# Performance work log

Measured on AMD Instinct MI355X. Metric: run time of the kernel, lower is better.

The kernel has to match this reference:

```python
import jax, jax.numpy as jnp
import numpy as np
from jax import lax

B_, L_, C_IN = 32, 1024, 3
D_MODEL, D_STATE, D_CONV, EXPAND = 256, 16, 4, 2
D_INNER = EXPAND * D_MODEL           # 512
DT_RANK = D_MODEL // 16              # 16
N_HEADS, N_CLASS = 8, 10
LN_EPS = 1e-5


def _pos_emb(L, d):
    pos = np.arange(L, dtype=np.float32)[:, None]
    div = np.exp(np.arange(0, d, 2, dtype=np.float32) * (-np.log(10000.0) / d))
    pe = np.zeros((L, d), np.float32)
    pe[:, 0::2] = np.sin(pos * div)
    pe[:, 1::2] = np.cos(pos * div)
    return jnp.asarray(pe)


def setup_inputs() -> dict:
    key = jax.random.key(0)
    ks = jax.random.split(key, 12)
    f = lambda k, shp, s: jax.random.normal(k, shp, jnp.float32) * s
    return {
        'x_enc': f(ks[0], (B_, L_, C_IN), 1.0),
        'x_mark_enc': jnp.ones((B_, L_), jnp.float32),
        'conv_emb_w': f(ks[1], (D_MODEL, C_IN, 3), (2.0 / (C_IN * 3)) ** 0.5),
        'in_proj_w': f(ks[2], (2 * D_INNER, D_MODEL), D_MODEL ** -0.5),
        'conv1d_w': f(ks[3], (D_INNER, 1, D_CONV), D_CONV ** -0.5),
        'conv1d_b': f(ks[4], (D_INNER,), 0.02),
        'x_proj_w': f(ks[5], (DT_RANK + 2 * D_STATE, D_INNER), D_INNER ** -0.5),
        'dt_proj_w': f(ks[6], (D_INNER, DT_RANK), DT_RANK ** -0.5),
        'dt_proj_b': f(ks[7], (D_INNER,), 0.1) - 2.0,
        'A_log': jnp.log(jnp.tile(jnp.arange(1, D_STATE + 1, dtype=jnp.float32), (D_INNER, 1))),
        'D': jnp.ones((D_INNER,), jnp.float32),
        'out_proj_w': f(ks[8], (D_MODEL, D_INNER), D_INNER ** -0.5),
        'ln_g': jnp.ones((D_MODEL,), jnp.float32),
        'ln_b': jnp.zeros((D_MODEL,), jnp.float32),
        'out_w': f(ks[9], (N_CLASS, D_MODEL), D_MODEL ** -0.5),
        'attn_w': f(ks[10], (N_HEADS, D_MODEL), 0.02),
        'attn_b': jnp.ones((N_HEADS,), jnp.float32),
    }


def _forward(x_enc, x_mark_enc, conv_emb_w, in_proj_w, conv1d_w, conv1d_b,
             x_proj_w, dt_proj_w, dt_proj_b, A_log, D, out_proj_w,
             ln_g, ln_b, out_w, attn_w, attn_b):
    silu = jax.nn.silu
    # --- embedding: Conv1d 'same' with replicate padding + sinusoidal PE ---
    xp = jnp.pad(x_enc, ((0, 0), (1, 1), (0, 0)), mode='edge')      # k=3 -> pad (1,1)
    x = lax.conv_general_dilated(xp.transpose(0, 2, 1), conv_emb_w, (1,), 'VALID',
                                 dimension_numbers=('NCH', 'OIH', 'NCH')).transpose(0, 2, 1)
    x = x + _pos_emb(L_, D_MODEL)[None]                              # (B,L,D)

    # --- Mamba_TimeVariant (standard Mamba selective scan) ---
    xz = jnp.einsum('bld,ed->ble', x, in_proj_w)                     # (B,L,2*Din)
    xin, z = xz[..., :D_INNER], xz[..., D_INNER:]
    # depthwise causal conv, kernel D_CONV
    xc = jnp.pad(xin.transpose(0, 2, 1), ((0, 0), (0, 0), (D_CONV - 1, 0)))
    xc = lax.conv_general_dilated(xc, conv1d_w, (1,), 'VALID',
                                  feature_group_count=D_INNER,
                                  dimension_numbers=('NCH', 'OIH', 'NCH'))
    xc = silu(xc.transpose(0, 2, 1) + conv1d_b)                      # (B,L,Din)

    dbl = jnp.einsum('bld,ed->ble', xc, x_proj_w)                    # (B,L,dt_rank+2*N)
    dtr = dbl[..., :DT_RANK]
    Bm = dbl[..., DT_RANK:DT_RANK + D_STATE]                         # (B,L,N)
    Cm = dbl[..., DT_RANK + D_STATE:]                                # (B,L,N)
    dt = jax.nn.softplus(jnp.einsum('blr,dr->bld', dtr, dt_proj_w) + dt_proj_b)
    A = -jnp.exp(A_log)                                              # (Din,N)

    def step(h, inp):
        dt_t, B_t, C_t, x_t = inp                                    # (B,Din),(B,N),(B,N),(B,Din)
        dA = jnp.exp(dt_t[..., None] * A)                            # (B,Din,N)
        h = dA * h + dt_t[..., None] * B_t[:, None, :] * x_t[..., None]
        y = jnp.einsum('bdn,bn->bd', h, C_t)
        return h, y

    h0 = jnp.zeros((B_, D_INNER, D_STATE), xc.dtype)
    inputs = (dt.transpose(1, 0, 2), Bm.transpose(1, 0, 2),
              Cm.transpose(1, 0, 2), xc.transpose(1, 0, 2))
    _, ys = lax.scan(step, h0, inputs)                               # (L,B,Din)
    y = ys.transpose(1, 0, 2) + xc * D                               # skip via D
    y = y * silu(z)
    m = jnp.einsum('bld,ed->ble', y, out_proj_w)                     # (B,L,Dmodel)

    # LayerNorm + SiLU
    mu = m.mean(-1, keepdims=True)
    var = ((m - mu) ** 2).mean(-1, keepdims=True)
    m = (m - mu) * lax.rsqrt(var + LN_EPS) * ln_g + ln_b
    m = silu(m)

    # classification head
    logit = jnp.einsum('bld,cd->blc', m, out_w) * x_mark_enc[..., None]
    s = jnp.einsum('bld,hd->blh', m, attn_w) + attn_b                # (B,L,H)
    w = jax.nn.softmax(jnp.max(s, axis=2, keepdims=True), axis=1)    # (B,L,1)
    return (logit * w).sum(1)                                        # (B,num_class)


def reference(x_enc, x_mark_enc, conv_emb_w, in_proj_w, conv1d_w, conv1d_b,
              x_proj_w, dt_proj_w, dt_proj_b, A_log, D, out_proj_w,
              ln_g, ln_b, out_w, attn_w, attn_b):
    return _forward(x_enc, x_mark_enc, conv_emb_w, in_proj_w, conv1d_w, conv1d_b,
                    x_proj_w, dt_proj_w, dt_proj_b, A_log, D, out_proj_w,
                    ln_g, ln_b, out_w, attn_w, attn_b)
```

## Files before the change

kernel.cpp:

```cpp
#include <hip/hip_runtime.h>
#include <hip/hip_bf16.h>
#include <math.h>

#define B_  32
#define L_  1024
#define CIN 3
#define DM  256
#define DI  512
#define NST 16
#define NH  8
#define NC  10
#define M_TOT (B_*L_)

typedef unsigned short u16;
typedef __attribute__((ext_vector_type(8))) short bf16x8;
typedef __attribute__((ext_vector_type(4))) float f32x4;

static __device__ __forceinline__ float sigmoidf_(float x) {
    return 1.0f / (1.0f + __expf(-x));
}
static __device__ __forceinline__ u16 f2bf(float f) {
    unsigned int u = __float_as_uint(f);
    return (u16)((u + 0x7FFF + ((u >> 16) & 1)) >> 16);
}
static __device__ __forceinline__ float bf2f(u16 u) {
    return __uint_as_float(((unsigned int)u) << 16);
}

static __device__ __forceinline__ void reduce16_quad(float& a, float& b,
                                                     float& c, float& d) {
    asm volatile(
        "s_nop 1\n\t"
        "v_add_f32 %0, %0, %0 quad_perm:[1,0,3,2] row_mask:0xf bank_mask:0xf\n\t"
        "v_add_f32 %1, %1, %1 quad_perm:[1,0,3,2] row_mask:0xf bank_mask:0xf\n\t"
        "v_add_f32 %2, %2, %2 quad_perm:[1,0,3,2] row_mask:0xf bank_mask:0xf\n\t"
        "v_add_f32 %3, %3, %3 quad_perm:[1,0,3,2] row_mask:0xf bank_mask:0xf\n\t"
        "v_add_f32 %0, %0, %0 quad_perm:[2,3,0,1] row_mask:0xf bank_mask:0xf\n\t"
        "v_add_f32 %1, %1, %1 quad_perm:[2,3,0,1] row_mask:0xf bank_mask:0xf\n\t"
        "v_add_f32 %2, %2, %2 quad_perm:[2,3,0,1] row_mask:0xf bank_mask:0xf\n\t"
        "v_add_f32 %3, %3, %3 quad_perm:[2,3,0,1] row_mask:0xf bank_mask:0xf\n\t"
        "v_add_f32 %0, %0, %0 row_ror:4 row_mask:0xf bank_mask:0xf\n\t"
        "v_add_f32 %1, %1, %1 row_ror:4 row_mask:0xf bank_mask:0xf\n\t"
        "v_add_f32 %2, %2, %2 row_ror:4 row_mask:0xf bank_mask:0xf\n\t"
        "v_add_f32 %3, %3, %3 row_ror:4 row_mask:0xf bank_mask:0xf\n\t"
        "v_add_f32 %0, %0, %0 row_ror:8 row_mask:0xf bank_mask:0xf\n\t"
        "v_add_f32 %1, %1, %1 row_ror:8 row_mask:0xf bank_mask:0xf\n\t"
        "v_add_f32 %2, %2, %2 row_ror:8 row_mask:0xf bank_mask:0xf\n\t"
        "v_add_f32 %3, %3, %3 row_ror:8 row_mask:0xf bank_mask:0xf\n\t"
        : "+v"(a), "+v"(b), "+v"(c), "+v"(d));
}

__global__ __launch_bounds__(256) void k_cvt(const float* __restrict__ in,
        u16* __restrict__ out) {
    int i = (blockIdx.x * 256 + threadIdx.x) * 4;
    float4 v = *(const float4*)(in + i);
    ushort4 o;
    o.x = f2bf(v.x); o.y = f2bf(v.y); o.z = f2bf(v.z); o.w = f2bf(v.w);
    *(ushort4*)(out + i) = o;
}

__global__ __launch_bounds__(256) void k_embed(const float* __restrict__ xe,
        const float* __restrict__ w, u16* __restrict__ x) {
    int bl = blockIdx.x;
    int l = bl & (L_-1);
    int b = bl >> 10;
    int d = threadIdx.x;
    const float* xb = xe + (size_t)b * L_ * CIN;
    int t0 = l > 0 ? l-1 : 0;
    int t2 = l < L_-1 ? l+1 : L_-1;
    const float* w3 = w + d*9;
    float acc = 0.f;
    #pragma unroll
    for (int i = 0; i < 3; ++i) {
        acc += xb[t0*3+i] * w3[i*3+0];
        acc += xb[l *3+i] * w3[i*3+1];
        acc += xb[t2*3+i] * w3[i*3+2];
    }
    int j = d >> 1;
    float div = expf((float)(2*j) * (-logf(10000.0f)/(float)DM));
    float ang = (float)l * div;
    acc += (d & 1) ? cosf(ang) : sinf(ang);
    x[(size_t)bl*DM + d] = f2bf(acc);
}

#define GST 40
__global__ __launch_bounds__(256) void k_gemm_mfma(
        const u16* __restrict__ A, const u16* __restrict__ W,
        float* __restrict__ O1, u16* __restrict__ O2b,
        int M, int N, int K, int S) {
    __shared__ u16 As[128*GST];
    __shared__ u16 Bs[128*GST];
    int tid = threadIdx.x;
    int row0 = blockIdx.y * 128, col0 = blockIdx.x * 128;
    int wave = tid >> 6, lane = tid & 63;
    int wr = (wave >> 1) * 64, wc = (wave & 1) * 64;
    int l16 = lane & 15, kl = lane >> 4;
    int srow = tid >> 1, skh = (tid & 1) * 16;
    const u16* Ag = A + (size_t)(row0 + srow) * K + skh;
    const u16* Wg = W + (size_t)(col0 + srow) * K + skh;

    f32x4 acc[4][4];
    #pragma unroll
    for (int m = 0; m < 4; ++m)
        #pragma unroll
        for (int n = 0; n < 4; ++n)
            acc[m][n] = (f32x4){0.f, 0.f, 0.f, 0.f};

    for (int k0 = 0; k0 < K; k0 += 32) {
        uint4 a0 = *(const uint4*)(Ag + k0);
        uint4 a1 = *(const uint4*)(Ag + k0 + 8);
        uint4 b0 = *(const uint4*)(Wg + k0);
        uint4 b1 = *(const uint4*)(Wg + k0 + 8);
        __syncthreads();
        *(uint4*)&As[srow*GST + skh]     = a0;
        *(uint4*)&As[srow*GST + skh + 8] = a1;
        *(uint4*)&Bs[srow*GST + skh]     = b0;
        *(uint4*)&Bs[srow*GST + skh + 8] = b1;
        __syncthreads();
        bf16x8 af[4], bf[4];
        #pragma unroll
        for (int m = 0; m < 4; ++m)
            af[m] = *(const bf16x8*)&As[(wr + m*16 + l16)*GST + kl*8];
        #pragma unroll
        for (int n = 0; n < 4; ++n)
            bf[n] = *(const bf16x8*)&Bs[(wc + n*16 + l16)*GST + kl*8];
        #pragma unroll
        for (int m = 0; m < 4; ++m)
            #pragma unroll
            for (int n = 0; n < 4; ++n)
                acc[m][n] = __builtin_amdgcn_mfma_f32_16x16x32_bf16(
                                af[m], bf[n], acc[m][n], 0, 0, 0);
    }

    #pragma unroll
    for (int m = 0; m < 4; ++m) {
        int rbase = row0 + wr + m*16 + kl*4;
        #pragma unroll
        for (int n = 0; n < 4; ++n) {
            int col = col0 + wc + n*16 + l16;
            #pragma unroll
            for (int r = 0; r < 4; ++r) {
                float v = acc[m][n][r];
                if (col < S) O1[(size_t)(rbase + r)*S + col] = v;
                else         O2b[(size_t)(rbase + r)*(N - S) + (col - S)] = f2bf(v);
            }
        }
    }
}

__global__ __launch_bounds__(256) void k_conv(const float* __restrict__ xin,
        const float* __restrict__ w, const float* __restrict__ bias,
        float* __restrict__ xc) {
    size_t i4 = (size_t)blockIdx.x * 256 + threadIdx.x;
    int d4 = (int)(i4 & (DI/4 - 1)) * 4;
    size_t m = i4 >> 7;
    int l = (int)(m & (L_-1));
    float4 wv0 = *(const float4*)(w + (size_t)(d4+0)*4);
    float4 wv1 = *(const float4*)(w + (size_t)(d4+1)*4);
    float4 wv2 = *(const float4*)(w + (size_t)(d4+2)*4);
    float4 wv3 = *(const float4*)(w + (size_t)(d4+3)*4);
    float W[4][4] = {{wv0.x,wv0.y,wv0.z,wv0.w},{wv1.x,wv1.y,wv1.z,wv1.w},
                     {wv2.x,wv2.y,wv2.z,wv2.w},{wv3.x,wv3.y,wv3.z,wv3.w}};
    float4 acc = *(const float4*)(bias + d4);
    #pragma unroll
    for (int k = 0; k < 4; ++k) {
        int t = l + k - 3;
        if (t >= 0) {
            float4 xv = *(const float4*)(xin + (m + k - 3)*DI + d4);
            acc.x = fmaf(xv.x, W[0][k], acc.x);
            acc.y = fmaf(xv.y, W[1][k], acc.y);
            acc.z = fmaf(xv.z, W[2][k], acc.z);
            acc.w = fmaf(xv.w, W[3][k], acc.w);
        }
    }
    float4 r;
    r.x = acc.x * sigmoidf_(acc.x);
    r.y = acc.y * sigmoidf_(acc.y);
    r.z = acc.z * sigmoidf_(acc.z);
    r.w = acc.w * sigmoidf_(acc.w);
    *(float4*)(xc + m*DI + d4) = r;
}

#define XBM 128
#define XBK 16
__global__ __launch_bounds__(256) void k_xproj(const float* __restrict__ xc,
        const float* __restrict__ wp, float* __restrict__ dbl) {
    __shared__ float As[XBK][XBM];
    __shared__ float Ws[XBK][48];
    int tid = threadIdx.x;
    int row0 = blockIdx.x * XBM;
    int lr = tid >> 1;
    int lk = (tid & 1) * 8;
    int we = tid >> 2;
    int wk = (tid & 3) * 4;
    int tx = tid & 15;
    int ty = tid >> 4;
    float acc[8][3];
    #pragma unroll
    for (int i = 0; i < 8; ++i)
        #pragma unroll
        for (int j = 0; j < 3; ++j) acc[i][j] = 0.f;

    for (int k0 = 0; k0 < DI; k0 += XBK) {
        float4 a0 = *(const float4*)(xc + (size_t)(row0+lr)*DI + k0 + lk);
        float4 a1 = *(const float4*)(xc + (size_t)(row0+lr)*DI + k0 + lk + 4);
        float4 w0 = make_float4(0.f,0.f,0.f,0.f);
        if (tid < 192) w0 = *(const float4*)(wp + (size_t)we*DI + k0 + wk);
        __syncthreads();
        As[lk+0][lr]=a0.x; As[lk+1][lr]=a0.y; As[lk+2][lr]=a0.z; As[lk+3][lr]=a0.w;
        As[lk+4][lr]=a1.x; As[lk+5][lr]=a1.y; As[lk+6][lr]=a1.z; As[lk+7][lr]=a1.w;
        if (tid < 192) {
            Ws[wk+0][we]=w0.x; Ws[wk+1][we]=w0.y; Ws[wk+2][we]=w0.z; Ws[wk+3][we]=w0.w;
        }
        __syncthreads();
        #pragma unroll
        for (int k = 0; k < XBK; ++k) {
            float4 av0 = *(const float4*)&As[k][ty*8];
            float4 av1 = *(const float4*)&As[k][ty*8+4];
            float w0_ = Ws[k][tx*3+0];
            float w1_ = Ws[k][tx*3+1];
            float w2_ = Ws[k][tx*3+2];
            float ar[8] = {av0.x,av0.y,av0.z,av0.w,av1.x,av1.y,av1.z,av1.w};
            #pragma unroll
            for (int i = 0; i < 8; ++i) {
                acc[i][0] = fmaf(ar[i], w0_, acc[i][0]);
                acc[i][1] = fmaf(ar[i], w1_, acc[i][1]);
                acc[i][2] = fmaf(ar[i], w2_, acc[i][2]);
            }
        }
    }
    #pragma unroll
    for (int i = 0; i < 8; ++i) {
        size_t r = row0 + ty*8 + i;
        #pragma unroll
        for (int j = 0; j < 3; ++j)
            dbl[r*48 + tx*3 + j] = acc[i][j];
    }
}

__global__ __launch_bounds__(256) void k_dtproj(const float* __restrict__ dbl,
        const float* __restrict__ dtw, const float* __restrict__ dtb,
        float* __restrict__ dt) {
    __shared__ float wl[DI][17];
    __shared__ float rl[32][16];
    size_t m0 = (size_t)blockIdx.x * 32;
    for (int i = threadIdx.x; i < DI*16; i += 256)
        wl[i >> 4][i & 15] = dtw[i];
    for (int i = threadIdx.x; i < 32*16; i += 256)
        rl[i >> 4][i & 15] = dbl[(m0 + (i>>4))*48 + (i & 15)];
    __syncthreads();
    float b0 = dtb[threadIdx.x];
    float b1 = dtb[256 + threadIdx.x];
    for (int mm = 0; mm < 32; ++mm) {
        #pragma unroll
        for (int half = 0; half < 2; ++half) {
            int d = half*256 + threadIdx.x;
            float acc = half ? b1 : b0;
            #pragma unroll
            for (int r = 0; r < 16; ++r)
                acc = fmaf(rl[mm][r], wl[d][r], acc);
            float sp = fmaxf(acc, 0.f) + log1pf(__expf(-fabsf(acc)));
            dt[(m0+mm)*DI + d] = sp;
        }
    }
}

#define SCAN_T 64
__global__ __launch_bounds__(256) void k_scan(const float* __restrict__ dt,
        const float* __restrict__ xc, const float* __restrict__ dbl,
        const float* __restrict__ A_log, const float* __restrict__ Dp,
        const u16* __restrict__ zbf, u16* __restrict__ ybf) {
    __shared__ float4 sq4[SCAN_T*17];

    int tid = threadIdx.x;
    int ch = tid >> 4;
    int n  = tid & 15;
    int d0 = blockIdx.x * 16;
    int b  = blockIdx.y;
    int d  = d0 + ch;
    float Avl2 = -expf(A_log[(size_t)d*NST + n]) * 1.44269504f;
    float h = 0.f;
    size_t base = (size_t)b * L_;

    int st = tid >> 2;
    int sc = (tid & 3) * 4;
    float4 Dv = *(const float4*)(Dp + d0 + sc);

    for (int t0 = 0; t0 < L_; t0 += SCAN_T) {
        __syncthreads();
        {
            size_t row = base + t0 + st;
            float4 dtv = *(const float4*)(dt + row*DI + d0 + sc);
            float4 xv  = *(const float4*)(xc + row*DI + d0 + sc);
            ushort4 zv4 = *(const ushort4*)(zbf + row*DI + d0 + sc);
            float z0 = bf2f(zv4.x), z1 = bf2f(zv4.y);
            float z2 = bf2f(zv4.z), z3 = bf2f(zv4.w);
            float g0 = z0 * sigmoidf_(z0);
            float g1 = z1 * sigmoidf_(z1);
            float g2 = z2 * sigmoidf_(z2);
            float g3 = z3 * sigmoidf_(z3);
            sq4[st*17 + sc+0] = make_float4(dtv.x, dtv.x*xv.x, xv.x*Dv.x*g0, g0);
            sq4[st*17 + sc+1] = make_float4(dtv.y, dtv.y*xv.y, xv.y*Dv.y*g1, g1);
            sq4[st*17 + sc+2] = make_float4(dtv.z, dtv.z*xv.z, xv.z*Dv.z*g2, g2);
            sq4[st*17 + sc+3] = make_float4(dtv.w, dtv.w*xv.w, xv.w*Dv.w*g3, g3);
        }
        __syncthreads();

        for (int tt = 0; tt < SCAN_T; tt += 16) {
            float Br[16], Cr[16];
            #pragma unroll
            for (int j = 0; j < 16; ++j) {
                size_t r48 = (base + t0 + tt + j) * 48;
                Br[j] = dbl[r48 + 16 + n];
                Cr[j] = dbl[r48 + 32 + n];
            }
            #pragma unroll
            for (int j4 = 0; j4 < 4; ++j4) {
                int tb = tt + j4*4;
                float4 q0 = sq4[(tb+0)*17 + ch];
                float4 q1 = sq4[(tb+1)*17 + ch];
                float4 q2 = sq4[(tb+2)*17 + ch];
                float4 q3 = sq4[(tb+3)*17 + ch];
                float dA;
                dA = exp2f(q0.x * Avl2);
                h = fmaf(dA, h, q0.y * Br[j4*4+0]);
                float p0 = h * Cr[j4*4+0];
                dA = exp2f(q1.x * Avl2);
                h = fmaf(dA, h, q1.y * Br[j4*4+1]);
                float p1 = h * Cr[j4*4+1];
                dA = exp2f(q2.x * Avl2);
                h = fmaf(dA, h, q2.y * Br[j4*4+2]);
                float p2 = h * Cr[j4*4+2];
                dA = exp2f(q3.x * Avl2);
                h = fmaf(dA, h, q3.y * Br[j4*4+3]);
                float p3 = h * Cr[j4*4+3];
                reduce16_quad(p0, p1, p2, p3);
                if (n == 0) {
                    size_t row = base + t0 + tb;
                    ybf[(row+0)*DI + d] = f2bf(fmaf(p0, q0.w, q0.z));
                    ybf[(row+1)*DI + d] = f2bf(fmaf(p1, q1.w, q1.z));
                    ybf[(row+2)*DI + d] = f2bf(fmaf(p2, q2.w, q2.z));
                    ybf[(row+3)*DI + d] = f2bf(fmaf(p3, q3.w, q3.z));
                }
            }
        }
    }
}

__global__ __launch_bounds__(256) void k_lnsilu(float* __restrict__ m,
        const float* __restrict__ g, const float* __restrict__ bta) {
    size_t row = (size_t)blockIdx.x*4 + (threadIdx.x >> 6);
    int lane = threadIdx.x & 63;
    float4 v = *(const float4*)(m + row*DM + lane*4);
    float s = v.x + v.y + v.z + v.w;
    #pragma unroll
    for (int o = 32; o > 0; o >>= 1) s += __shfl_xor(s, o);
    float mu = s * (1.0f/DM);
    float4 c = make_float4(v.x-mu, v.y-mu, v.z-mu, v.w-mu);
    float s2 = c.x*c.x + c.y*c.y + c.z*c.z + c.w*c.w;
    #pragma unroll
    for (int o = 32; o > 0; o >>= 1) s2 += __shfl_xor(s2, o);
    float rstd = 1.0f / sqrtf(s2 * (1.0f/DM) + 1e-5f);
    float4 gv = *(const float4*)(g + lane*4);
    float4 bv = *(const float4*)(bta + lane*4);
    float o0 = c.x*rstd*gv.x + bv.x;
    float o1 = c.y*rstd*gv.y + bv.y;
    float o2 = c.z*rstd*gv.z + bv.z;
    float o3 = c.w*rstd*gv.w + bv.w;
    float4 r;
    r.x = o0 * sigmoidf_(o0);
    r.y = o1 * sigmoidf_(o1);
    r.z = o2 * sigmoidf_(o2);
    r.w = o3 * sigmoidf_(o3);
    *(float4*)(m + row*DM + lane*4) = r;
}

#define HBK 32
__global__ __launch_bounds__(256) void k_heads18(const float* __restrict__ m,
        const float* __restrict__ aw, const float* __restrict__ ow,
        float* __restrict__ r18) {
    __shared__ float As[128][36];
    __shared__ float Ws[18][36];
    int tid = threadIdx.x;
    int row0 = blockIdx.x * 128;
    int r = tid >> 1, ch = tid & 1, cb = ch * 9;
    int sr = tid >> 1, sk = (tid & 1) * 16;
    float acc[9];
    #pragma unroll
    for (int c = 0; c < 9; ++c) acc[c] = 0.f;

    for (int k0 = 0; k0 < DM; k0 += HBK) {
        float4 a[4];
        #pragma unroll
        for (int q = 0; q < 4; ++q)
            a[q] = *(const float4*)(m + (size_t)(row0+sr)*DM + k0 + sk + q*4);
        float4 wv = make_float4(0.f,0.f,0.f,0.f);
        int wc = tid >> 3, wk = (tid & 7) * 4;
        if (tid < 144) {
            const float* wsrc = (wc < NH) ? (aw + wc*DM) : (ow + (wc-NH)*DM);
            wv = *(const float4*)(wsrc + k0 + wk);
        }
        __syncthreads();
        #pragma unroll
        for (int q = 0; q < 4; ++q)
            *(float4*)&As[sr][sk + q*4] = a[q];
        if (tid < 144)
            *(float4*)&Ws[wc][wk] = wv;
        __syncthreads();
        #pragma unroll
        for (int k4 = 0; k4 < HBK/4; ++k4) {
            float4 av = *(const float4*)&As[r][k4*4];
            #pragma unroll
            for (int c = 0; c < 9; ++c) {
                float4 w4 = *(const float4*)&Ws[cb + c][k4*4];
                acc[c] += av.x*w4.x + av.y*w4.y + av.z*w4.z + av.w*w4.w;
            }
        }
        __syncthreads();
    }
    #pragma unroll
    for (int c = 0; c < 9; ++c)
        r18[(size_t)(row0 + r)*18 + cb + c] = acc[c];
}

__global__ __launch_bounds__(256) void k_final(const float* __restrict__ r18,
        const float* __restrict__ ab, const float* __restrict__ xmark,
        float* __restrict__ out) {
    __shared__ float e[L_];
    __shared__ float red[256];
    int b = blockIdx.x;
    int tid = threadIdx.x;
    float abr[NH];
    #pragma unroll
    for (int j = 0; j < NH; ++j) abr[j] = ab[j];
    float mx = -1e30f;
    for (int l = tid; l < L_; l += 256) {
        const float* rr = r18 + ((size_t)b*L_ + l)*18;
        float sm = rr[0] + abr[0];
        #pragma unroll
        for (int j = 1; j < NH; ++j) sm = fmaxf(sm, rr[j] + abr[j]);
        e[l] = sm;
        mx = fmaxf(mx, sm);
    }
    #pragma unroll
    for (int o = 32; o > 0; o >>= 1) mx = fmaxf(mx, __shfl_xor(mx, o));
    red[tid] = mx;
    __syncthreads();
    mx = fmaxf(fmaxf(red[0], red[64]), fmaxf(red[128], red[192]));
    __syncthreads();
    float ssum = 0.f;
    for (int l = tid; l < L_; l += 256) {
        float ev = __expf(e[l] - mx);
        e[l] = ev;
        ssum += ev;
    }
    #pragma unroll
    for (int o = 32; o > 0; o >>= 1) ssum += __shfl_xor(ssum, o);
    if ((tid & 63) == 0) red[tid >> 6] = ssum;
    __syncthreads();
    float inv = 1.0f / (red[0]+red[1]+red[2]+red[3]);
    float acc[NC];
    #pragma unroll
    for (int c = 0; c < NC; ++c) acc[c] = 0.f;
    for (int l = tid; l < L_; l += 256) {
        float wl = e[l] * xmark[(size_t)b*L_ + l];
        const float* lg = r18 + ((size_t)b*L_ + l)*18 + NH;
        #pragma unroll
        for (int c = 0; c < NC; ++c) acc[c] = fmaf(wl, lg[c], acc[c]);
    }
    __syncthreads();
    for (int c = 0; c < NC; ++c) {
        red[tid] = acc[c];
        __syncthreads();
        if (tid < 64) {
            float s2 = red[tid]+red[tid+64]+red[tid+128]+red[tid+192];
            #pragma unroll
            for (int o = 32; o > 0; o >>= 1) s2 += __shfl_xor(s2, o);
            if (tid == 0) out[(size_t)b*NC + c] = s2 * inv;
        }
        __syncthreads();
    }
}

extern "C" void kernel_launch(void* const* d_in, const int* in_sizes, int n_in,
                              void* d_out, int out_size, void* d_ws, size_t ws_size,
                              hipStream_t stream) {
    const float* x_enc  = (const float*)d_in[0];
    const float* x_mark = (const float*)d_in[1];
    const float* cemb_w = (const float*)d_in[2];
    const float* inp_w  = (const float*)d_in[3];
    const float* c1_w   = (const float*)d_in[4];
    const float* c1_b   = (const float*)d_in[5];
    const float* xp_w   = (const float*)d_in[6];
    const float* dtp_w  = (const float*)d_in[7];
    const float* dtp_b  = (const float*)d_in[8];
    const float* A_log  = (const float*)d_in[9];
    const float* Dp     = (const float*)d_in[10];
    const float* outp_w = (const float*)d_in[11];
    const float* ln_g   = (const float*)d_in[12];
    const float* ln_b   = (const float*)d_in[13];
    const float* out_w  = (const float*)d_in[14];
    const float* attn_w = (const float*)d_in[15];
    const float* attn_b = (const float*)d_in[16];
    float* out = (float*)d_out;

    char* ws = (char*)d_ws;
    size_t o = 0;
    u16*   xbf  = (u16*)(ws + o);  o += (size_t)M_TOT*DM*2;
    float* xin  = (float*)(ws + o); o += (size_t)M_TOT*DI*4;
    u16*   zbf  = (u16*)(ws + o);  o += (size_t)M_TOT*DI*2;
    float* xc   = (float*)(ws + o); o += (size_t)M_TOT*DI*4;
    u16*   ybf  = (u16*)(ws + o);  o += (size_t)M_TOT*DI*2;
    float* dbl  = (float*)(ws + o); o += (size_t)M_TOT*48*4;
    u16*   wbfi = (u16*)(ws + o);  o += (size_t)2*DI*DM*2;
    u16*   wbfo = (u16*)(ws + o);  o += (size_t)DM*DI*2;
    float* r18  = (float*)(ws + o); o += (size_t)M_TOT*18*4;
    float* dt = xin;
    float* mm = xc;

    k_cvt   <<<(2*DI*DM)/1024, 256, 0, stream>>>(inp_w, wbfi);
    k_cvt   <<<(DM*DI)/1024, 256, 0, stream>>>(outp_w, wbfo);
    k_embed <<<M_TOT, 256, 0, stream>>>(x_enc, cemb_w, xbf);
    k_gemm_mfma<<<dim3(8, M_TOT/128), 256, 0, stream>>>(xbf, wbfi, xin, zbf,
                                                        M_TOT, 2*DI, DM, DI);
    k_conv  <<<(M_TOT*DI/4)/256, 256, 0, stream>>>(xin, c1_w, c1_b, xc);
    k_xproj <<<M_TOT/XBM, 256, 0, stream>>>(xc, xp_w, dbl);
    k_dtproj<<<M_TOT/32, 256, 0, stream>>>(dbl, dtp_w, dtp_b, dt);
    k_scan  <<<dim3(DI/16, B_), 256, 0, stream>>>(dt, xc, dbl, A_log, Dp, zbf, ybf);
    k_gemm_mfma<<<dim3(2, M_TOT/128), 256, 0, stream>>>(ybf, wbfo, mm, zbf,
                                                        M_TOT, DM, DI, DM);
    k_lnsilu<<<M_TOT/4, 256, 0, stream>>>(mm, ln_g, ln_b);
    k_heads18<<<M_TOT/128, 256, 0, stream>>>(mm, attn_w, out_w, r18);
    k_final <<<B_, 256, 0, stream>>>(r18, attn_b, x_mark, out);
}
```

Measured before the change: 475.0 us.

## Transpose B/C projections to state-major layout and spread scan output stores

```diff
diff --git a/kernel.cpp b/kernel.cpp
--- a/kernel.cpp
+++ b/kernel.cpp
@@ -184,7 +184,8 @@
 #define XBM 128
 #define XBK 16
 __global__ __launch_bounds__(256) void k_xproj(const float* __restrict__ xc,
-        const float* __restrict__ wp, float* __restrict__ dbl) {
+        const float* __restrict__ wp, float* __restrict__ dbl,
+        float* __restrict__ BT, float* __restrict__ CT) {
     __shared__ float As[XBK][XBM];
     __shared__ float Ws[XBK][48];
     int tid = threadIdx.x;
@@ -233,8 +234,13 @@
     for (int i = 0; i < 8; ++i) {
         size_t r = row0 + ty*8 + i;
         #pragma unroll
-        for (int j = 0; j < 3; ++j)
-            dbl[r*48 + tx*3 + j] = acc[i][j];
+        for (int j = 0; j < 3; ++j) {
+            int c = tx*3 + j;
+            float v = acc[i][j];
+            if (c < 16)      dbl[r*48 + c] = v;
+            else if (c < 32) BT[(size_t)(c-16)*M_TOT + r] = v;
+            else             CT[(size_t)(c-32)*M_TOT + r] = v;
+        }
     }
 }
 
@@ -267,9 +273,10 @@
 
 #define SCAN_T 64
 __global__ __launch_bounds__(256) void k_scan(const float* __restrict__ dt,
-        const float* __restrict__ xc, const float* __restrict__ dbl,
-        const float* __restrict__ A_log, const float* __restrict__ Dp,
-        const u16* __restrict__ zbf, u16* __restrict__ ybf) {
+        const float* __restrict__ xc, const float* __restrict__ BT,
+        const float* __restrict__ CT, const float* __restrict__ A_log,
+        const float* __restrict__ Dp, const u16* __restrict__ zbf,
+        u16* __restrict__ ybf) {
     __shared__ float4 sq4[SCAN_T*17];
 
     int tid = threadIdx.x;
@@ -281,6 +288,8 @@
     float Avl2 = -expf(A_log[(size_t)d*NST + n]) * 1.44269504f;
     float h = 0.f;
     size_t base = (size_t)b * L_;
+    const float* BTn = BT + (size_t)n * M_TOT + base;
+    const float* CTn = CT + (size_t)n * M_TOT + base;
 
     int st = tid >> 2;
     int sc = (tid & 3) * 4;
@@ -307,13 +316,13 @@
         __syncthreads();
 
         for (int tt = 0; tt < SCAN_T; tt += 16) {
-            float Br[16], Cr[16];
-            #pragma unroll
-            for (int j = 0; j < 16; ++j) {
-                size_t r48 = (base + t0 + tt + j) * 48;
-                Br[j] = dbl[r48 + 16 + n];
-                Cr[j] = dbl[r48 + 32 + n];
+            float4 Bv[4], Cv[4];
+            #pragma unroll
+            for (int q = 0; q < 4; ++q) {
+                Bv[q] = *(const float4*)(BTn + t0 + tt + q*4);
+                Cv[q] = *(const float4*)(CTn + t0 + tt + q*4);
             }
+            float yreg = 0.f;
             #pragma unroll
             for (int j4 = 0; j4 < 4; ++j4) {
                 int tb = tt + j4*4;
@@ -321,28 +330,33 @@
                 float4 q1 = sq4[(tb+1)*17 + ch];
                 float4 q2 = sq4[(tb+2)*17 + ch];
                 float4 q3 = sq4[(tb+3)*17 + ch];
+                const float* Bp = (const float*)&Bv[j4];
+                const float* Cp = (const float*)&Cv[j4];
                 float dA;
                 dA = exp2f(q0.x * Avl2);
-                h = fmaf(dA, h, q0.y * Br[j4*4+0]);
-                float p0 = h * Cr[j4*4+0];
+                h = fmaf(dA, h, q0.y * Bp[0]);
+                float p0 = h * Cp[0];
                 dA = exp2f(q1.x * Avl2);
-                h = fmaf(dA, h, q1.y * Br[j4*4+1]);
-                float p1 = h * Cr[j4*4+1];
+                h = fmaf(dA, h, q1.y * Bp[1]);
+                float p1 = h * Cp[1];
                 dA = exp2f(q2.x * Avl2);
-                h = fmaf(dA, h, q2.y * Br[j4*4+2]);
-                float p2 = h * Cr[j4*4+2];
+                h = fmaf(dA, h, q2.y * Bp[2]);
+                float p2 = h * Cp[2];
                 dA = exp2f(q3.x * Avl2);
-                h = fmaf(dA, h, q3.y * Br[j4*4+3]);
-                float p3 = h * Cr[j4*4+3];
+                h = fmaf(dA, h, q3.y * Bp[3]);
+                float p3 = h * Cp[3];
                 reduce16_quad(p0, p1, p2, p3);
-                if (n == 0) {
-                    size_t row = base + t0 + tb;
-                    ybf[(row+0)*DI + d] = f2bf(fmaf(p0, q0.w, q0.z));
-                    ybf[(row+1)*DI + d] = f2bf(fmaf(p1, q1.w, q1.z));
-                    ybf[(row+2)*DI + d] = f2bf(fmaf(p2, q2.w, q2.z));
-                    ybf[(row+3)*DI + d] = f2bf(fmaf(p3, q3.w, q3.z));
-                }
+                float y0 = fmaf(p0, q0.w, q0.z);
+                float y1 = fmaf(p1, q1.w, q1.z);
+                float y2 = fmaf(p2, q2.w, q2.z);
+                float y3 = fmaf(p3, q3.w, q3.z);
+                int rel = n - j4*4;
+                yreg = (rel == 0) ? y0 : yreg;
+                yreg = (rel == 1) ? y1 : yreg;
+                yreg = (rel == 2) ? y2 : yreg;
+                yreg = (rel == 3) ? y3 : yreg;
             }
+            ybf[(base + t0 + tt + n)*DI + d] = f2bf(yreg);
         }
     }
 }
@@ -512,6 +526,8 @@
     float* xc   = (float*)(ws + o); o += (size_t)M_TOT*DI*4;
     u16*   ybf  = (u16*)(ws + o);  o += (size_t)M_TOT*DI*2;
     float* dbl  = (float*)(ws + o); o += (size_t)M_TOT*48*4;
+    float* BT   = (float*)(ws + o); o += (size_t)NST*M_TOT*4;
+    float* CT   = (float*)(ws + o); o += (size_t)NST*M_TOT*4;
     u16*   wbfi = (u16*)(ws + o);  o += (size_t)2*DI*DM*2;
     u16*   wbfo = (u16*)(ws + o);  o += (size_t)DM*DI*2;
     float* r18  = (float*)(ws + o); o += (size_t)M_TOT*18*4;
@@ -524,9 +540,10 @@
     k_gemm_mfma<<<dim3(8, M_TOT/128), 256, 0, stream>>>(xbf, wbfi, xin, zbf,
                                                         M_TOT, 2*DI, DM, DI);
     k_conv  <<<(M_TOT*DI/4)/256, 256, 0, stream>>>(xin, c1_w, c1_b, xc);
-    k_xproj <<<M_TOT/XBM, 256, 0, stream>>>(xc, xp_w, dbl);
+    k_xproj <<<M_TOT/XBM, 256, 0, stream>>>(xc, xp_w, dbl, BT, CT);
     k_dtproj<<<M_TOT/32, 256, 0, stream>>>(dbl, dtp_w, dtp_b, dt);
-    k_scan  <<<dim3(DI/16, B_), 256, 0, stream>>>(dt, xc, dbl, A_log, Dp, zbf, ybf);
+    k_scan  <<<dim3(DI/16, B_), 256, 0, stream>>>(dt, xc, BT, CT, A_log, Dp,
+                                                  zbf, ybf);
     k_gemm_mfma<<<dim3(2, M_TOT/128), 256, 0, stream>>>(ybf, wbfo, mm, zbf,
                                                         M_TOT, DM, DI, DM);
     k_lnsilu<<<M_TOT/4, 256, 0, stream>>>(mm, ln_g, ln_b);
```

After: 560.5 us. 18.0% more time.
